# Kernel tuning notes

Hardware: AMD Instinct MI355X
Metric: run time of the kernel (lower is better)

The kernel has to match this reference:

```python
import jax, jax.numpy as jnp
import numpy as np

B, S, D, H = 4, 1024, 1024, 16
HD = D // H
EPS = 1e-5


def _layernorm(x, g, b):
    m = jnp.mean(x, axis=-1, keepdims=True)
    v = jnp.mean((x - m) ** 2, axis=-1, keepdims=True)
    return (x - m) * jax.lax.rsqrt(v + EPS) * g + b


def setup_inputs() -> dict:
    key = jax.random.key(0)
    ks = jax.random.split(key, 8)
    sc = 1.0 / np.sqrt(D)
    return {
        "x": jax.random.normal(ks[0], (B, S, D), dtype=jnp.float32),
        "seq_len": jax.random.randint(ks[1], (B,), 1, S + 1, dtype=jnp.int32),
        "Wq": jax.random.normal(ks[2], (D, D), dtype=jnp.float32) * sc,
        "bq": jnp.zeros((D,), dtype=jnp.float32),
        "Wk": jax.random.normal(ks[3], (D, D), dtype=jnp.float32) * sc,
        "bk": jnp.zeros((D,), dtype=jnp.float32),
        "Wv": jax.random.normal(ks[4], (D, D), dtype=jnp.float32) * sc,
        "bv": jnp.zeros((D,), dtype=jnp.float32),
        "ln_g": jnp.ones((HD,), dtype=jnp.float32),
        "ln_b": jnp.zeros((HD,), dtype=jnp.float32),
    }


def reference(x, seq_len, Wq, bq, Wk, bk, Wv, bv, ln_g, ln_b):
    # Faithful quirk: k and v are projections of the ALREADY projected q.
    q = x @ Wq.T + bq                      # [B,S,D]
    k = q @ Wk.T + bk
    v = q @ Wv.T + bv
    # [B,S,D] -> [B,H,S,HD]
    def split_heads(t):
        return t.reshape(B, S, H, HD).transpose(0, 2, 1, 3)
    q, k, v = split_heads(q), split_heads(k), split_heads(v)
    # shared per-head LayerNorm over head_dim
    q = _layernorm(q, ln_g, ln_b)
    k = _layernorm(k, ln_g, ln_b)
    v = _layernorm(v, ln_g, ln_b)
    # raw scores (no temperature scaling in the original; temperature=1.0 unused)
    scores = jnp.einsum("bhqd,bhkd->bhqk", q, k)
    # encoder_mask: multiplicative validity mask on key positions, repeated per head
    mask = (jnp.arange(S)[None, :] < seq_len[:, None]).astype(scores.dtype)  # [B,S]
    scores = scores * mask[:, None, None, :]
    attn = jax.nn.softmax(scores, axis=-1)
    # dropout is identity at inference
    out = jnp.einsum("bhqk,bhkd->bhqd", attn, v)
    return out.transpose(0, 2, 1, 3).reshape(B, S, D)
```

## Files before the change

kernel.cpp:

```cpp
#include <hip/hip_runtime.h>

#define B_  4
#define S_  1024
#define D_  1024
#define H_  16
#define HD_ 64
#define EPS_ 1e-5f

typedef _Float16 f16x8 __attribute__((ext_vector_type(8)));
typedef _Float16 f16x4 __attribute__((ext_vector_type(4)));
typedef __bf16 bf16x8 __attribute__((ext_vector_type(8)));
typedef float  f32x4  __attribute__((ext_vector_type(4)));
typedef unsigned short ushort4v __attribute__((ext_vector_type(4)));

#define GLD16(gp, lp) __builtin_amdgcn_global_load_lds( \
    (const __attribute__((address_space(1))) void*)(gp), \
    (__attribute__((address_space(3))) void*)(lp), 16, 0, 0)

static __device__ __forceinline__ unsigned pk2bf(float a, float b) {
  union { __bf16 h; unsigned short u; } ua, ub;
  ua.h = (__bf16)a; ub.h = (__bf16)b;
  return (unsigned)ua.u | ((unsigned)ub.u << 16);
}

__global__ __launch_bounds__(256) void cvt_all(
    const float* __restrict__ x,  _Float16* __restrict__ xh,
    const float* __restrict__ Wq, _Float16* __restrict__ wqh,
    const float* __restrict__ Wk, _Float16* __restrict__ wkh,
    const float* __restrict__ Wv, _Float16* __restrict__ wvh,
    float* __restrict__ Vtail) {
  int bid = blockIdx.x;
  if (bid >= 7168) {
    int i = (bid - 7168) * 1024 + threadIdx.x * 4;
    *(float4*)(Vtail + i) = make_float4(0.f, 0.f, 0.f, 0.f);
    return;
  }
  const float* src; _Float16* dst; int base;
  if (bid < 4096)      { src = x;  dst = xh;  base = bid; }
  else if (bid < 5120) { src = Wq; dst = wqh; base = bid - 4096; }
  else if (bid < 6144) { src = Wk; dst = wkh; base = bid - 5120; }
  else                 { src = Wv; dst = wvh; base = bid - 6144; }
  int i = base * 1024 + threadIdx.x * 4;
  float4 f = *(const float4*)(src + i);
  f16x4 h;
  h.x = (_Float16)f.x; h.y = (_Float16)f.y; h.z = (_Float16)f.z; h.w = (_Float16)f.w;
  *(f16x4*)(dst + i) = h;
}

__global__ __launch_bounds__(256, 2) void gemm_q_ln(
    const _Float16* __restrict__ A,
    const _Float16* __restrict__ Bw,
    const float* __restrict__ bias,
    const float* __restrict__ ln_g, const float* __restrict__ ln_b,
    _Float16* __restrict__ qh,
    _Float16* __restrict__ Qn)
{
  __shared__ _Float16 As[4 * 128 * 32];
  __shared__ _Float16 Bs[4 * 64 * 32];

  int tid  = threadIdx.x;
  int lane = tid & 63;
  int wave = tid >> 6;
  int qd = lane >> 4, l15 = lane & 15;

  int flat = blockIdx.x + 16 * blockIdx.y;
  int swz  = (flat & 7) * 64 + (flat >> 3);
  int bx = swz & 15, by = swz >> 4;

  long row0 = (long)by * 128;
  long col0 = (long)bx * 64;

  int r_a = tid >> 2;
  int c_a = (tid & 3) * 8;

  f32x4 acc[2][4] = {};

  for (int kk = 0; kk < D_; kk += 128) {
    for (int ks2 = 0; ks2 < 4; ks2++) {
      GLD16(A  + (row0 + r_a) * D_ + kk + ks2 * 32 + c_a,      As + ks2 * 4096 + tid * 8);
      GLD16(A  + (row0 + 64 + r_a) * D_ + kk + ks2 * 32 + c_a, As + ks2 * 4096 + 2048 + tid * 8);
      GLD16(Bw + (col0 + r_a) * D_ + kk + ks2 * 32 + c_a,      Bs + ks2 * 2048 + tid * 8);
    }
    __syncthreads();

    for (int ks = 0; ks < 4; ks++) {
      f16x8 af[2], bfr[4];
      for (int i = 0; i < 2; i++)
        af[i]  = *(const f16x8*)(As + ks * 4096 + (wave * 32 + i * 16 + l15) * 32 + qd * 8);
      for (int j = 0; j < 4; j++)
        bfr[j] = *(const f16x8*)(Bs + ks * 2048 + (j * 16 + l15) * 32 + qd * 8);
      for (int i = 0; i < 2; i++)
        for (int j = 0; j < 4; j++)
          acc[i][j] = __builtin_amdgcn_mfma_f32_16x16x32_f16(af[i], bfr[j], acc[i][j], 0, 0, 0);
    }
    __syncthreads();
  }

  int h = bx;
  long rw = row0 + wave * 32;
  int bb = (int)(rw >> 10);
  long bh = (long)bb * H_ + h;
  float gv[4], bl[4], bc[4];
  for (int j = 0; j < 4; j++) {
    int d = j * 16 + l15;
    gv[j] = ln_g[d]; bl[j] = ln_b[d]; bc[j] = bias[h * 64 + d];
  }
  for (int i = 0; i < 2; i++) {
    float m4[4], i4[4];
    for (int r = 0; r < 4; r++) {
      float s = 0.f, q = 0.f;
      for (int j = 0; j < 4; j++) {
        float y = acc[i][j][r] + bc[j];
        s += y; q = fmaf(y, y, q);
      }
      for (int off = 1; off < 16; off <<= 1) {
        s += __shfl_xor(s, off, 64);
        q += __shfl_xor(q, off, 64);
      }
      float m = s * (1.f / 64.f);
      m4[r] = m;
      i4[r] = rsqrtf(q * (1.f / 64.f) - m * m + EPS_);
    }
    for (int r = 0; r < 4; r++) {
      long srow = rw + i * 16 + qd * 4 + r;
      long sloc = srow & (S_ - 1);
      for (int j = 0; j < 4; j++) {
        float y = acc[i][j][r] + bc[j];
        qh[srow * D_ + h * 64 + j * 16 + l15] = (_Float16)y;
        Qn[(bh * S_ + sloc) * HD_ + j * 16 + l15] =
            (_Float16)((y - m4[r]) * i4[r] * gv[j] + bl[j]);
      }
    }
  }
}

__global__ __launch_bounds__(256, 2) void gemm_kv_ln(
    const _Float16* __restrict__ A,
    const _Float16* __restrict__ Bk, const float* __restrict__ bk,
    const _Float16* __restrict__ Bv, const float* __restrict__ bv,
    const float* __restrict__ ln_g, const float* __restrict__ ln_b,
    const int* __restrict__ seq_len,
    _Float16* __restrict__ Kn,
    unsigned short* __restrict__ Vt,
    float* __restrict__ Vtail)
{
  __shared__ _Float16 As[4 * 128 * 32];
  __shared__ _Float16 Bs[4 * 128 * 32];

  int tid  = threadIdx.x;
  int lane = tid & 63;
  int wave = tid >> 6;
  int wm = wave >> 1, wn = wave & 1;
  int qd = lane >> 4, l15 = lane & 15;

  int flat = blockIdx.x + 8 * blockIdx.y + 256 * blockIdx.z;
  int swz  = (flat & 7) * 64 + (flat >> 3);
  int z    = swz >> 8;
  int rem  = swz & 255;
  int by   = rem >> 3, bx = rem & 7;

  const _Float16* Bm = z ? Bv : Bk;
  const float* bias  = z ? bv : bk;

  long row0 = (long)by * 128;
  long col0 = (long)bx * 128;

  int r_a = tid >> 2;
  int c_a = (tid & 3) * 8;

  f32x4 acc[4][4] = {};

  for (int kk = 0; kk < D_; kk += 128) {
    for (int ks2 = 0; ks2 < 4; ks2++) {
      GLD16(A  + (row0 + r_a) * D_ + kk + ks2 * 32 + c_a,      As + ks2 * 4096 + tid * 8);
      GLD16(A  + (row0 + 64 + r_a) * D_ + kk + ks2 * 32 + c_a, As + ks2 * 4096 + 2048 + tid * 8);
      GLD16(Bm + (col0 + r_a) * D_ + kk + ks2 * 32 + c_a,      Bs + ks2 * 4096 + tid * 8);
      GLD16(Bm + (col0 + 64 + r_a) * D_ + kk + ks2 * 32 + c_a, Bs + ks2 * 4096 + 2048 + tid * 8);
    }
    __syncthreads();

    for (int ks = 0; ks < 4; ks++) {
      f16x8 af[4], bfr[4];
      for (int t = 0; t < 4; t++) {
        af[t]  = *(const f16x8*)(As + ks * 4096 + (wm * 64 + t * 16 + l15) * 32 + qd * 8);
        bfr[t] = *(const f16x8*)(Bs + ks * 4096 + (wn * 64 + t * 16 + l15) * 32 + qd * 8);
      }
      for (int i = 0; i < 4; i++)
        for (int j = 0; j < 4; j++)
          acc[i][j] = __builtin_amdgcn_mfma_f32_16x16x32_f16(af[i], bfr[j], acc[i][j], 0, 0, 0);
    }
    __syncthreads();
  }

  int h = bx * 2 + wn;
  long rw = row0 + wm * 64;
  int bb = (int)(rw >> 10);
  long bh = (long)bb * H_ + h;
  float gv[4], bl[4], bc[4];
  for (int j = 0; j < 4; j++) {
    int d = j * 16 + l15;
    gv[j] = ln_g[d]; bl[j] = ln_b[d]; bc[j] = bias[h * 64 + d];
  }

  if (z == 0) {
    for (int i = 0; i < 4; i++) {
      float m4[4], i4[4];
      for (int r = 0; r < 4; r++) {
        float s = 0.f, q = 0.f;
        for (int j = 0; j < 4; j++) {
          float y = acc[i][j][r] + bc[j];
          s += y; q = fmaf(y, y, q);
        }
        for (int off = 1; off < 16; off <<= 1) {
          s += __shfl_xor(s, off, 64);
          q += __shfl_xor(q, off, 64);
        }
        float m = s * (1.f / 64.f);
        m4[r] = m;
        i4[r] = rsqrtf(q * (1.f / 64.f) - m * m + EPS_);
      }
      for (int r = 0; r < 4; r++) {
        long sloc = (rw + i * 16 + qd * 4 + r) & (S_ - 1);
        for (int j = 0; j < 4; j++) {
          float y = acc[i][j][r] + bc[j];
          Kn[(bh * S_ + sloc) * HD_ + j * 16 + l15] =
              (_Float16)((y - m4[r]) * i4[r] * gv[j] + bl[j]);
        }
      }
    }
  } else {
    int len = seq_len[bb];
    float tsum[4] = {0.f, 0.f, 0.f, 0.f};
    for (int i = 0; i < 4; i++) {
      float m4[4], i4[4];
      for (int r = 0; r < 4; r++) {
        float s = 0.f, q = 0.f;
        for (int j = 0; j < 4; j++) {
          float y = acc[i][j][r] + bc[j];
          s += y; q = fmaf(y, y, q);
        }
        for (int off = 1; off < 16; off <<= 1) {
          s += __shfl_xor(s, off, 64);
          q += __shfl_xor(q, off, 64);
        }
        float m = s * (1.f / 64.f);
        m4[r] = m;
        i4[r] = rsqrtf(q * (1.f / 64.f) - m * m + EPS_);
      }
      int s0loc = (int)((rw + i * 16 + qd * 4) & (S_ - 1));
      for (int j = 0; j < 4; j++) {
        ushort4v w;
        for (int r = 0; r < 4; r++) {
          float y = acc[i][j][r] + bc[j];
          float vo = (y - m4[r]) * i4[r] * gv[j] + bl[j];
          __bf16 vb = (__bf16)vo;
          union { __bf16 hh; unsigned short uu; } cv; cv.hh = vb;
          w[r] = cv.uu;
          if (s0loc + r >= len) tsum[j] += (float)vb;
        }
        *(ushort4v*)(Vt + (bh * HD_ + j * 16 + l15) * S_ + s0loc) = w;
      }
    }
    if (((int)(rw & (S_ - 1)) + 64) > len)
      for (int j = 0; j < 4; j++)
        atomicAdd(&Vtail[bh * HD_ + j * 16 + l15], tsum[j]);
  }
}

__global__ __launch_bounds__(256, 4) void attn(
    const _Float16* __restrict__ Qn,
    const _Float16* __restrict__ Kn,
    const unsigned short* __restrict__ Vt,
    const float* __restrict__ Vtail,
    const int* __restrict__ seq_len,
    float* __restrict__ out)
{
  __shared__ _Float16 Ks[2][64 * 32];
  __shared__ unsigned short Vts[2][64 * 32];
  __shared__ unsigned int Pt[4][16 * 36];

  int tid = threadIdx.x, lane = tid & 63, wave = tid >> 6;
  int qd = lane >> 4, l15 = lane & 15;
  int b = blockIdx.x;
  int h = blockIdx.y;
  int q0 = blockIdx.z * 64;
  long bh = (long)b * H_ + h;
  int len = seq_len[b];
  int ntile = (len + 63) >> 6;

  int skey = tid >> 2;
  int schunk = (tid & 3) * 8;

  f16x8 qf[2];
  {
    const _Float16* qp = Qn + (bh * S_ + q0 + wave * 16 + l15) * HD_;
    qf[0] = *(const f16x8*)(qp + qd * 8);
    qf[1] = *(const f16x8*)(qp + 32 + qd * 8);
  }
  f32x4 tv[4];
  for (int t = 0; t < 4; t++)
    tv[t] = *(const f32x4*)(Vtail + bh * HD_ + t * 16 + qd * 4);

  f32x4 o[4] = {};
  float den = 0.f;

  unsigned int* pw = &Pt[wave][0];

  for (int kt = 0; kt < ntile; kt++) {
    GLD16(Kn + (bh * S_ + kt * 64 + skey) * HD_ + schunk,      &Ks[0][0] + tid * 8);
    GLD16(Kn + (bh * S_ + kt * 64 + skey) * HD_ + 32 + schunk, &Ks[1][0] + tid * 8);
    GLD16(Vt + (bh * HD_ + skey) * S_ + kt * 64 + schunk,      &Vts[0][0] + tid * 8);
    GLD16(Vt + (bh * HD_ + skey) * S_ + kt * 64 + 32 + schunk, &Vts[1][0] + tid * 8);
    __syncthreads();

    f32x4 sacc[4] = {};
    for (int tn = 0; tn < 4; tn++) {
      f16x8 kf0 = *(const f16x8*)(&Ks[0][0] + (tn * 16 + l15) * 32 + qd * 8);
      f16x8 kf1 = *(const f16x8*)(&Ks[1][0] + (tn * 16 + l15) * 32 + qd * 8);
      sacc[tn] = __builtin_amdgcn_mfma_f32_16x16x32_f16(kf0, qf[0], sacc[tn], 0, 0, 0);
      sacc[tn] = __builtin_amdgcn_mfma_f32_16x16x32_f16(kf1, qf[1], sacc[tn], 0, 0, 0);
    }

    if (kt * 64 + 64 <= len) {
      for (int tn = 0; tn < 4; tn++) {
        float p0 = __expf(sacc[tn][0]);
        float p1 = __expf(sacc[tn][1]);
        float p2 = __expf(sacc[tn][2]);
        float p3 = __expf(sacc[tn][3]);
        unsigned w0 = pk2bf(p0, p1);
        unsigned w1 = pk2bf(p2, p3);
        den += (float)(__bf16)p0 + (float)(__bf16)p1
             + (float)(__bf16)p2 + (float)(__bf16)p3;
        *(uint2*)(pw + l15 * 36 + tn * 8 + qd * 2) = make_uint2(w0, w1);
      }
    } else {
      for (int tn = 0; tn < 4; tn++) {
        int kg = kt * 64 + tn * 16 + qd * 4;
        float p[4];
        for (int r = 0; r < 4; r++)
          p[r] = (kg + r < len) ? __expf(sacc[tn][r]) : 0.f;
        unsigned w0 = pk2bf(p[0], p[1]);
        unsigned w1 = pk2bf(p[2], p[3]);
        den += (float)(__bf16)p[0] + (float)(__bf16)p[1]
             + (float)(__bf16)p[2] + (float)(__bf16)p[3];
        *(uint2*)(pw + l15 * 36 + tn * 8 + qd * 2) = make_uint2(w0, w1);
      }
    }

    bf16x8 pf0 = *(const bf16x8*)((const unsigned short*)pw + l15 * 72 + qd * 8);
    bf16x8 pf1 = *(const bf16x8*)((const unsigned short*)pw + l15 * 72 + 32 + qd * 8);
    for (int t = 0; t < 4; t++) {
      bf16x8 vf0 = *(const bf16x8*)(&Vts[0][0] + (t * 16 + l15) * 32 + qd * 8);
      bf16x8 vf1 = *(const bf16x8*)(&Vts[1][0] + (t * 16 + l15) * 32 + qd * 8);
      o[t] = __builtin_amdgcn_mfma_f32_16x16x32_bf16(vf0, pf0, o[t], 0, 0, 0);
      o[t] = __builtin_amdgcn_mfma_f32_16x16x32_bf16(vf1, pf1, o[t], 0, 0, 0);
    }
    __syncthreads();
  }

  den += __shfl_xor(den, 16, 64);
  den += __shfl_xor(den, 32, 64);
  den += (float)(S_ - len);

  long s = q0 + wave * 16 + l15;
  float* op = out + ((long)b * S_ + s) * D_ + h * 64 + qd * 4;
  for (int t = 0; t < 4; t++) {
    f32x4 r;
    for (int rr = 0; rr < 4; rr++)
      r[rr] = (o[t][rr] + tv[t][rr]) / den;
    *(f32x4*)(op + t * 16) = r;
  }
}

extern "C" void kernel_launch(void* const* d_in, const int* in_sizes, int n_in,
                              void* d_out, int out_size, void* d_ws, size_t ws_size,
                              hipStream_t stream) {
  const float* x     = (const float*)d_in[0];
  const int*  seq    = (const int*)d_in[1];
  const float* Wq    = (const float*)d_in[2];
  const float* bq    = (const float*)d_in[3];
  const float* Wk    = (const float*)d_in[4];
  const float* bk    = (const float*)d_in[5];
  const float* Wv    = (const float*)d_in[6];
  const float* bv    = (const float*)d_in[7];
  const float* ln_g  = (const float*)d_in[8];
  const float* ln_b  = (const float*)d_in[9];
  float* out = (float*)d_out;

  char* ws = (char*)d_ws;
  _Float16* xh  = (_Float16*)(ws);
  _Float16* wqh = (_Float16*)(ws + (8l  << 20));
  _Float16* wkh = (_Float16*)(ws + (10l << 20));
  _Float16* wvh = (_Float16*)(ws + (12l << 20));
  float*    Vtail = (float*)(ws + (14l << 20));
  _Float16* qh  = (_Float16*)(ws + (16l << 20));
  _Float16* Qn  = (_Float16*)(ws + (40l << 20));
  _Float16* Kn  = (_Float16*)(ws + (48l << 20));
  unsigned short* Vt = (unsigned short*)(ws + (56l << 20));

  cvt_all<<<7172, 256, 0, stream>>>(x, xh, Wq, wqh, Wk, wkh, Wv, wvh, Vtail);

  dim3 g1(D_ / 64, (B_ * S_) / 128);
  gemm_q_ln<<<g1, 256, 0, stream>>>(xh, wqh, bq, ln_g, ln_b, qh, Qn);

  dim3 g2(D_ / 128, (B_ * S_) / 128, 2);
  gemm_kv_ln<<<g2, 256, 0, stream>>>(qh, wkh, bk, wvh, bv, ln_g, ln_b, seq,
                                     Kn, Vt, Vtail);

  dim3 g4(B_, H_, S_ / 64);
  attn<<<g4, 256, 0, stream>>>(Qn, Kn, Vt, Vtail, seq, out);
}
```

Baseline: 163.2 us.

## Give each attention wave two 16-row query tiles and halve the block size

The attention kernel now runs 2 waves (128 threads) per 64-query block, and each wave processes 32 query rows as two 16-row MFMA tiles. Each K/V fragment read from LDS is reused across both tiles, and each thread issues two async global-to-LDS loads per buffer. The goal is to cut LDS read traffic and per-block overhead per unit of MFMA work. The cost is more registers per thread and half as many waves per block to hide latency, with launch bounds changed to (128,3).

```diff
diff --git a/kernel.cpp b/kernel.cpp
--- a/kernel.cpp
+++ b/kernel.cpp
@@ -267,7 +267,7 @@
   }
 }
 
-__global__ __launch_bounds__(256, 4) void attn(
+__global__ __launch_bounds__(128, 3) void attn(
     const _Float16* __restrict__ Qn,
     const _Float16* __restrict__ Kn,
     const unsigned short* __restrict__ Vt,
@@ -277,7 +277,7 @@
 {
   __shared__ _Float16 Ks[2][64 * 32];
   __shared__ unsigned short Vts[2][64 * 32];
-  __shared__ unsigned int Pt[4][16 * 36];
+  __shared__ unsigned int Pt[2][32 * 36];
 
   int tid = threadIdx.x, lane = tid & 63, wave = tid >> 6;
   int qd = lane >> 4, l15 = lane & 15;
@@ -288,87 +288,100 @@
   int len = seq_len[b];
   int ntile = (len + 63) >> 6;
 
-  int skey = tid >> 2;
-  int schunk = (tid & 3) * 8;
-
-  f16x8 qf[2];
-  {
-    const _Float16* qp = Qn + (bh * S_ + q0 + wave * 16 + l15) * HD_;
-    qf[0] = *(const f16x8*)(qp + qd * 8);
-    qf[1] = *(const f16x8*)(qp + 32 + qd * 8);
+  f16x8 qf[2][2];
+  for (int mt = 0; mt < 2; mt++) {
+    const _Float16* qp = Qn + (bh * S_ + q0 + wave * 32 + mt * 16 + l15) * HD_;
+    qf[mt][0] = *(const f16x8*)(qp + qd * 8);
+    qf[mt][1] = *(const f16x8*)(qp + 32 + qd * 8);
   }
   f32x4 tv[4];
   for (int t = 0; t < 4; t++)
     tv[t] = *(const f32x4*)(Vtail + bh * HD_ + t * 16 + qd * 4);
 
-  f32x4 o[4] = {};
-  float den = 0.f;
+  f32x4 o[2][4] = {};
+  float den[2] = {0.f, 0.f};
 
   unsigned int* pw = &Pt[wave][0];
 
   for (int kt = 0; kt < ntile; kt++) {
-    GLD16(Kn + (bh * S_ + kt * 64 + skey) * HD_ + schunk,      &Ks[0][0] + tid * 8);
-    GLD16(Kn + (bh * S_ + kt * 64 + skey) * HD_ + 32 + schunk, &Ks[1][0] + tid * 8);
-    GLD16(Vt + (bh * HD_ + skey) * S_ + kt * 64 + schunk,      &Vts[0][0] + tid * 8);
-    GLD16(Vt + (bh * HD_ + skey) * S_ + kt * 64 + 32 + schunk, &Vts[1][0] + tid * 8);
-    __syncthreads();
-
-    f32x4 sacc[4] = {};
+    for (int p = tid; p < 256; p += 128) {
+      GLD16(Kn + (bh * S_ + kt * 64 + (p >> 2)) * HD_ + (p & 3) * 8,      &Ks[0][0] + p * 8);
+      GLD16(Kn + (bh * S_ + kt * 64 + (p >> 2)) * HD_ + 32 + (p & 3) * 8, &Ks[1][0] + p * 8);
+      GLD16(Vt + (bh * HD_ + (p >> 2)) * S_ + kt * 64 + (p & 3) * 8,      &Vts[0][0] + p * 8);
+      GLD16(Vt + (bh * HD_ + (p >> 2)) * S_ + kt * 64 + 32 + (p & 3) * 8, &Vts[1][0] + p * 8);
+    }
+    __syncthreads();
+
+    f32x4 sacc[2][4] = {};
     for (int tn = 0; tn < 4; tn++) {
       f16x8 kf0 = *(const f16x8*)(&Ks[0][0] + (tn * 16 + l15) * 32 + qd * 8);
       f16x8 kf1 = *(const f16x8*)(&Ks[1][0] + (tn * 16 + l15) * 32 + qd * 8);
-      sacc[tn] = __builtin_amdgcn_mfma_f32_16x16x32_f16(kf0, qf[0], sacc[tn], 0, 0, 0);
-      sacc[tn] = __builtin_amdgcn_mfma_f32_16x16x32_f16(kf1, qf[1], sacc[tn], 0, 0, 0);
+      for (int mt = 0; mt < 2; mt++) {
+        sacc[mt][tn] = __builtin_amdgcn_mfma_f32_16x16x32_f16(kf0, qf[mt][0], sacc[mt][tn], 0, 0, 0);
+        sacc[mt][tn] = __builtin_amdgcn_mfma_f32_16x16x32_f16(kf1, qf[mt][1], sacc[mt][tn], 0, 0, 0);
+      }
     }
 
     if (kt * 64 + 64 <= len) {
-      for (int tn = 0; tn < 4; tn++) {
-        float p0 = __expf(sacc[tn][0]);
-        float p1 = __expf(sacc[tn][1]);
-        float p2 = __expf(sacc[tn][2]);
-        float p3 = __expf(sacc[tn][3]);
-        unsigned w0 = pk2bf(p0, p1);
-        unsigned w1 = pk2bf(p2, p3);
-        den += (float)(__bf16)p0 + (float)(__bf16)p1
-             + (float)(__bf16)p2 + (float)(__bf16)p3;
-        *(uint2*)(pw + l15 * 36 + tn * 8 + qd * 2) = make_uint2(w0, w1);
-      }
+      for (int mt = 0; mt < 2; mt++)
+        for (int tn = 0; tn < 4; tn++) {
+          float p0 = __expf(sacc[mt][tn][0]);
+          float p1 = __expf(sacc[mt][tn][1]);
+          float p2 = __expf(sacc[mt][tn][2]);
+          float p3 = __expf(sacc[mt][tn][3]);
+          unsigned w0 = pk2bf(p0, p1);
+          unsigned w1 = pk2bf(p2, p3);
+          den[mt] += (float)(__bf16)p0 + (float)(__bf16)p1
+                   + (float)(__bf16)p2 + (float)(__bf16)p3;
+          *(uint2*)(pw + (mt * 16 + l15) * 36 + tn * 8 + qd * 2) = make_uint2(w0, w1);
+        }
     } else {
-      for (int tn = 0; tn < 4; tn++) {
-        int kg = kt * 64 + tn * 16 + qd * 4;
-        float p[4];
-        for (int r = 0; r < 4; r++)
-          p[r] = (kg + r < len) ? __expf(sacc[tn][r]) : 0.f;
-        unsigned w0 = pk2bf(p[0], p[1]);
-        unsigned w1 = pk2bf(p[2], p[3]);
-        den += (float)(__bf16)p[0] + (float)(__bf16)p[1]
-             + (float)(__bf16)p[2] + (float)(__bf16)p[3];
-        *(uint2*)(pw + l15 * 36 + tn * 8 + qd * 2) = make_uint2(w0, w1);
-      }
-    }
-
-    bf16x8 pf0 = *(const bf16x8*)((const unsigned short*)pw + l15 * 72 + qd * 8);
-    bf16x8 pf1 = *(const bf16x8*)((const unsigned short*)pw + l15 * 72 + 32 + qd * 8);
+      for (int mt = 0; mt < 2; mt++)
+        for (int tn = 0; tn < 4; tn++) {
+          int kg = kt * 64 + tn * 16 + qd * 4;
+          float p[4];
+          for (int r = 0; r < 4; r++)
+            p[r] = (kg + r < len) ? __expf(sacc[mt][tn][r]) : 0.f;
+          unsigned w0 = pk2bf(p[0], p[1]);
+          unsigned w1 = pk2bf(p[2], p[3]);
+          den[mt] += (float)(__bf16)p[0] + (float)(__bf16)p[1]
+                   + (float)(__bf16)p[2] + (float)(__bf16)p[3];
+          *(uint2*)(pw + (mt * 16 + l15) * 36 + tn * 8 + qd * 2) = make_uint2(w0, w1);
+        }
+    }
+
+    bf16x8 pf[2][2];
+    for (int mt = 0; mt < 2; mt++) {
+      pf[mt][0] = *(const bf16x8*)((const unsigned short*)pw + (mt * 16 + l15) * 72 + qd * 8);
+      pf[mt][1] = *(const bf16x8*)((const unsigned short*)pw + (mt * 16 + l15) * 72 + 32 + qd * 8);
+    }
     for (int t = 0; t < 4; t++) {
       bf16x8 vf0 = *(const bf16x8*)(&Vts[0][0] + (t * 16 + l15) * 32 + qd * 8);
       bf16x8 vf1 = *(const bf16x8*)(&Vts[1][0] + (t * 16 + l15) * 32 + qd * 8);
-      o[t] = __builtin_amdgcn_mfma_f32_16x16x32_bf16(vf0, pf0, o[t], 0, 0, 0);
-      o[t] = __builtin_amdgcn_mfma_f32_16x16x32_bf16(vf1, pf1, o[t], 0, 0, 0);
-    }
-    __syncthreads();
-  }
-
-  den += __shfl_xor(den, 16, 64);
-  den += __shfl_xor(den, 32, 64);
-  den += (float)(S_ - len);
-
-  long s = q0 + wave * 16 + l15;
-  float* op = out + ((long)b * S_ + s) * D_ + h * 64 + qd * 4;
-  for (int t = 0; t < 4; t++) {
-    f32x4 r;
-    for (int rr = 0; rr < 4; rr++)
-      r[rr] = (o[t][rr] + tv[t][rr]) / den;
-    *(f32x4*)(op + t * 16) = r;
+      for (int mt = 0; mt < 2; mt++) {
+        o[mt][t] = __builtin_amdgcn_mfma_f32_16x16x32_bf16(vf0, pf[mt][0], o[mt][t], 0, 0, 0);
+        o[mt][t] = __builtin_amdgcn_mfma_f32_16x16x32_bf16(vf1, pf[mt][1], o[mt][t], 0, 0, 0);
+      }
+    }
+    __syncthreads();
+  }
+
+  float tden = (float)(S_ - len);
+  for (int mt = 0; mt < 2; mt++) {
+    den[mt] += __shfl_xor(den[mt], 16, 64);
+    den[mt] += __shfl_xor(den[mt], 32, 64);
+    den[mt] += tden;
+  }
+
+  for (int mt = 0; mt < 2; mt++) {
+    long s = q0 + wave * 32 + mt * 16 + l15;
+    float* op = out + ((long)b * S_ + s) * D_ + h * 64 + qd * 4;
+    for (int t = 0; t < 4; t++) {
+      f32x4 r;
+      for (int rr = 0; rr < 4; rr++)
+        r[rr] = (o[mt][t][rr] + tv[t][rr]) / den[mt];
+      *(f32x4*)(op + t * 16) = r;
+    }
   }
 }
 
@@ -408,5 +421,5 @@
                                      Kn, Vt, Vtail);
 
   dim3 g4(B_, H_, S_ / 64);
-  attn<<<g4, 256, 0, stream>>>(Qn, Kn, Vt, Vtail, seq, out);
-}
+  attn<<<g4, 128, 0, stream>>>(Qn, Kn, Vt, Vtail, seq, out);
+}
```

After: 166.7 us. 1.02x slower.
